# Kernel tuning notes

Hardware: AMD Instinct MI355X
Metric: run time of the kernel (lower is better)

Reference implementation:

```python
import jax, jax.numpy as jnp
import numpy as np

B = 4          # batch_size (config.batch_size)
N = 17000      # num_prots (nodes per graph)
F_IN = 256     # num_features
C = 128        # out_channels
E = 2176000    # num edges (avg degree 32)
NODES = B * N


def _gcn_layer(x, W, b, src, dst, n):
    """PyG GCNConv: add self-loops, sym-normalized aggregation, then bias.
    out[i] = sum_{j->i} d_j^{-1/2} d_i^{-1/2} (x_j W) + d_i^{-1} (x_i W) + b
    with d = degree(dst) + 1 (self loop)."""
    h = x @ W  # [n, C]
    deg = jax.ops.segment_sum(jnp.ones(src.shape[0], x.dtype), dst, num_segments=n) + 1.0
    dinv = jax.lax.rsqrt(deg)  # [n]
    coef = dinv[src] * dinv[dst]                      # [E]
    agg = jax.ops.segment_sum(h[src] * coef[:, None], dst, num_segments=n)
    agg = agg + h * (dinv * dinv)[:, None]            # self-loop term
    return agg + b


def setup_inputs() -> dict:
    key = jax.random.key(0)
    ks = jax.random.split(key, 16)

    def glorot(k, shape):
        fan_in, fan_out = shape[0], shape[1]
        s = jnp.sqrt(6.0 / (fan_in + fan_out))
        return jax.random.uniform(k, shape, jnp.float32, -s, s)

    inp = {
        "x": jax.random.normal(ks[0], (NODES, F_IN), jnp.float32),
        "edge_index": jax.random.randint(ks[1], (2, E), 0, NODES, jnp.int32),
        "protein_mask": jax.random.randint(ks[2], (B, N), 0, 2, jnp.int32),
        "W1": glorot(ks[3], (F_IN, C)), "b1": jnp.zeros((C,), jnp.float32),
        "W2": glorot(ks[4], (C, C)),    "b2": jnp.zeros((C,), jnp.float32),
        "W3": glorot(ks[5], (C, C)),    "b3": jnp.zeros((C,), jnp.float32),
        "lw1": glorot(ks[6], (C, 256)), "lb1": jnp.zeros((256,), jnp.float32),
        "lw2": glorot(ks[7], (256, 64)), "lb2": jnp.zeros((64,), jnp.float32),
        "lw3": glorot(ks[8], (64, 16)),  "lb3": jnp.zeros((16,), jnp.float32),
        "lw4": glorot(ks[9], (16, 1)),   "lb4": jnp.zeros((1,), jnp.float32),
    }
    return inp


def reference(x, edge_index, protein_mask, W1, b1, W2, b2, W3, b3,
              lw1, lb1, lw2, lb2, lw3, lb3, lw4, lb4):
    src, dst = edge_index[0], edge_index[1]
    h1 = jax.nn.relu(_gcn_layer(x, W1, b1, src, dst, NODES))   # [NODES, C]
    h2 = jax.nn.relu(_gcn_layer(h1, W2, b2, src, dst, NODES))
    h3 = jax.nn.relu(_gcn_layer(h2, W3, b3, src, dst, NODES))
    s = (h1 + h2 + h3).reshape(B, N, C)                        # residual sum
    mask = protein_mask.astype(jnp.float32)                    # [B, N]
    pooled = jnp.einsum('bn,bnc->bc', mask, s)                 # masked bmm pool [B, C]
    z = jax.nn.relu(pooled @ lw1 + lb1)
    z = jax.nn.relu(z @ lw2 + lb2)
    z = jax.nn.relu(z @ lw3 + lb3)
    return z @ lw4 + lb4                                       # [B, 1]
```

## Files before the change

kernel.cpp:

```cpp
#include <hip/hip_runtime.h>
#include <hip/hip_bf16.h>
#include <cstdint>

#define F_IN 256
#define C 128
#define NBUK_MAX 320
#define CHUNK 4096
#define CAP 12288

typedef short bf8_t __attribute__((ext_vector_type(8)));
typedef float f4_t  __attribute__((ext_vector_type(4)));

static inline size_t align256(size_t x) { return (x + 255) & ~(size_t)255; }

static __device__ inline unsigned pack_bf16(float a, float b) {
    __hip_bfloat162 h = __float22bfloat162_rn(make_float2(a, b));
    return *(unsigned*)&h;
}

static __device__ inline bf8_t pack8(float4 u0, float4 u1) {
    union { unsigned u[4]; bf8_t v; } r;
    r.u[0] = pack_bf16(u0.x, u0.y);
    r.u[1] = pack_bf16(u0.z, u0.w);
    r.u[2] = pack_bf16(u1.x, u1.y);
    r.u[3] = pack_bf16(u1.z, u1.w);
    return r.v;
}

__global__ __launch_bounds__(512) void part_gemm1_kernel(
        const int* __restrict__ src, const int* __restrict__ dst,
        int* __restrict__ cntb, int* __restrict__ ebuf, int E, int nblk_part,
        const float* __restrict__ X, const __hip_bfloat16* __restrict__ Wsw,
        __hip_bfloat16* __restrict__ G, int M) {
    __shared__ __align__(16) char smem[36864];
    const int tid = threadIdx.x;

    if ((int)blockIdx.x < nblk_part) {
        int* hist = (int*)smem;
        int* base = hist + NBUK_MAX;
        int* gbase = base + NBUK_MAX;
        int2* stage = (int2*)(smem + 4096);
        const int e0 = blockIdx.x * CHUNK;
        const int cnt = min(CHUNK, E - e0);

        for (int i = tid; i < NBUK_MAX; i += 512) hist[i] = 0;
        __syncthreads();

        int2 ev[CHUNK / 512];
        int mo[CHUNK / 512];
#pragma unroll
        for (int k = 0; k < CHUNK / 512; ++k) {
            int e = e0 + k * 512 + tid;
            if (e < E) {
                int2 v;
                v.x = src[e];
                v.y = dst[e];
                ev[k] = v;
                mo[k] = atomicAdd(&hist[v.y >> 8], 1);
            }
        }
        __syncthreads();
        if (tid < 64) {
            int acc[5];
            int s = 0;
#pragma unroll
            for (int j = 0; j < 5; ++j) {
                acc[j] = s;
                s += hist[tid * 5 + j];
            }
            int tot = s;
#pragma unroll
            for (int d = 1; d < 64; d <<= 1) {
                int o = __shfl_up(tot, d);
                if (tid >= d) tot += o;
            }
            int excl = tot - s;
#pragma unroll
            for (int j = 0; j < 5; ++j) base[tid * 5 + j] = excl + acc[j];
        }
        __syncthreads();
        for (int i = tid; i < NBUK_MAX; i += 512) {
            int h = hist[i];
            gbase[i] = h ? atomicAdd(&cntb[i], h) : 0;
        }
        __syncthreads();
#pragma unroll
        for (int k = 0; k < CHUNK / 512; ++k) {
            int e = e0 + k * 512 + tid;
            if (e < E) stage[base[ev[k].y >> 8] + mo[k]] = ev[k];
        }
        __syncthreads();
        for (int i = tid; i < cnt; i += 512) {
            int2 e = stage[i];
            int b = e.y >> 8;
            ebuf[(size_t)b * CAP + gbase[b] + (i - base[b])] = ((e.y & 255) << 24) | e.x;
        }
    } else {
        char* lds = smem;
        const int gb = blockIdx.x - nblk_part;
        const int l = tid & 63;
        const int w = tid >> 6;
        const int lm = l & 15;
        const int lk = (l >> 4) * 8;
        const int row0 = gb * 128 + w * 16;
        const int K = F_IN;

        f4_t acc[8] = {};
        const int r = min(row0 + lm, M - 1);
        const float* xf = X + (size_t)r * K + lk;

        for (int c = 0; c < 2; ++c) {
            if (c) __syncthreads();
            const char* wsrc = (const char*)Wsw + (size_t)c * 32768;
            for (int o = tid * 16; o < 32768; o += 512 * 16)
                *(uint4*)(lds + o) = *(const uint4*)(wsrc + o);
            __syncthreads();
#pragma unroll
            for (int s2 = 0; s2 < 4; ++s2) {
                const int s = c * 4 + s2;
                float4 u0 = *(const float4*)(xf + s * 32);
                float4 u1 = *(const float4*)(xf + s * 32 + 4);
                bf8_t a = pack8(u0, u1);
                const char* bbase = lds + ((size_t)(s2 * 8) * 64 + l) * 16;
#pragma unroll
                for (int u = 0; u < 8; ++u) {
                    bf8_t b = *(const bf8_t*)(bbase + (size_t)u * 64 * 16);
                    acc[u] = __builtin_amdgcn_mfma_f32_16x16x32_bf16(a, b, acc[u], 0, 0, 0);
                }
            }
        }
        const int rbase = row0 + (l >> 4) * 4;
#pragma unroll
        for (int rr = 0; rr < 4; ++rr) {
            int row = rbase + rr;
            if (row < M) {
#pragma unroll
                for (int u = 0; u < 8; ++u)
                    G[(size_t)row * C + u * 16 + lm] = __float2bfloat16(acc[u][rr]);
            }
        }
    }
}

__global__ __launch_bounds__(256) void csr_build_kernel(const int* __restrict__ ebuf,
                                                        const int* __restrict__ cntb,
                                                        int nbuk,
                                                        int* __restrict__ offs,
                                                        float* __restrict__ dinv,
                                                        int* __restrict__ csr, int nodes) {
    __shared__ int hist[NBUK_MAX];
    __shared__ int basep[NBUK_MAX];
    __shared__ int deg[256];
    __shared__ int p[256];
    __shared__ int pre[257];
    __shared__ int cur[256];
    const int b = blockIdx.x;
    const int n0 = b << 8;
    const int ncnt = min(256, nodes - n0);
    const int tid = threadIdx.x;

    for (int bk = tid; bk < NBUK_MAX; bk += 256)
        hist[bk] = (bk < nbuk) ? cntb[bk] : 0;
    __syncthreads();
    if (tid < 64) {
        int acc[5];
        int s = 0;
#pragma unroll
        for (int j = 0; j < 5; ++j) {
            acc[j] = s;
            s += hist[tid * 5 + j];
        }
        int tot = s;
#pragma unroll
        for (int d = 1; d < 64; d <<= 1) {
            int o = __shfl_up(tot, d);
            if (tid >= d) tot += o;
        }
        int excl = tot - s;
#pragma unroll
        for (int j = 0; j < 5; ++j) basep[tid * 5 + j] = excl + acc[j];
    }
    __syncthreads();
    const int eb = basep[b];
    const int cntE = hist[b];
    const int* slab = ebuf + (size_t)b * CAP;

    deg[tid] = 0;
    __syncthreads();
    for (int k = tid; k < cntE; k += 256)
        atomicAdd(&deg[(unsigned)slab[k] >> 24], 1);
    __syncthreads();
    p[tid] = deg[tid];
    __syncthreads();
    for (int d = 1; d < 256; d <<= 1) {
        int v = (tid >= d) ? p[tid - d] : 0;
        __syncthreads();
        p[tid] += v;
        __syncthreads();
    }
    pre[tid + 1] = p[tid];
    if (tid == 0) pre[0] = 0;
    __syncthreads();

    for (int i = tid; i <= ncnt; i += 256)
        offs[n0 + i] = eb + pre[i] + n0 + i;
    if (tid < ncnt) {
        dinv[n0 + tid] = rsqrtf((float)(deg[tid] + 1));
        csr[eb + pre[tid] + n0 + tid] = n0 + tid;
    }
    cur[tid] = 0;
    __syncthreads();
    for (int k = tid; k < cntE; k += 256) {
        int v = slab[k];
        int loc = (unsigned)v >> 24;
        int q = atomicAdd(&cur[loc], 1);
        csr[eb + pre[loc] + n0 + loc + 1 + q] = v & 0xFFFFFF;
    }
}

static __device__ inline void swz_one(const float* __restrict__ W,
                                      __hip_bfloat16* __restrict__ Wsw, int i) {
    int l = i & 63;
    int u = (i >> 6) & 7;
    int t = i >> 9;
    int krow = t * 32 + (l >> 4) * 8;
    int col = u * 16 + (l & 15);
    unsigned packed[4];
#pragma unroll
    for (int j = 0; j < 4; ++j) {
        float a = W[(size_t)(krow + 2 * j) * C + col];
        float b = W[(size_t)(krow + 2 * j + 1) * C + col];
        packed[j] = pack_bf16(a, b);
    }
    uint4 o = make_uint4(packed[0], packed[1], packed[2], packed[3]);
    *(uint4*)(Wsw + (size_t)i * 8) = o;
}

__global__ __launch_bounds__(256) void wswz_all_kernel(const float* __restrict__ W1,
                                                       const float* __restrict__ W2,
                                                       const float* __restrict__ W3,
                                                       __hip_bfloat16* __restrict__ Wsw1,
                                                       __hip_bfloat16* __restrict__ Wsw2,
                                                       __hip_bfloat16* __restrict__ Wsw3,
                                                       int* __restrict__ cntb, int nbuk,
                                                       float* __restrict__ pooled) {
    if (blockIdx.x == 32) {
        const int tid = threadIdx.x;
        for (int i = tid; i < nbuk; i += 256) cntb[i] = 0;
        for (int i = tid; i < 4 * C; i += 256) pooled[i] = 0.f;
        return;
    }
    int i = blockIdx.x * blockDim.x + threadIdx.x;
    if (i < 4096)      swz_one(W1, Wsw1, i);
    else if (i < 6144) swz_one(W2, Wsw2, i - 4096);
    else if (i < 8192) swz_one(W3, Wsw3, i - 6144);
}

__global__ __launch_bounds__(256) void mfma_gemm_kernel(const __hip_bfloat16* __restrict__ Xv,
                                                        const __hip_bfloat16* __restrict__ Wsw,
                                                        const float* __restrict__ dinv,
                                                        __hip_bfloat16* __restrict__ G,
                                                        int M) {
    __shared__ char lds[32768];
    const int tid = threadIdx.x;
    const int l = tid & 63;
    const int w = tid >> 6;
    const int lm = l & 15;
    const int lk = (l >> 4) * 8;
    const int row0 = blockIdx.x * 128 + w * 32;
    const int K = C;

    f4_t acc[2][8] = {};
    const __hip_bfloat16* xb[2];
#pragma unroll
    for (int mt = 0; mt < 2; ++mt) {
        int r = min(row0 + mt * 16 + lm, M - 1);
        xb[mt] = Xv + (size_t)r * K + lk;
    }
    bf8_t cb[2];
#pragma unroll
    for (int mt = 0; mt < 2; ++mt)
        cb[mt] = *(const bf8_t*)(xb[mt]);

    for (int o = tid * 16; o < 32768; o += 256 * 16)
        *(uint4*)(lds + o) = *(const uint4*)((const char*)Wsw + o);
    __syncthreads();

    for (int s = 0; s < 4; ++s) {
        bf8_t nb[2];
        if (s + 1 < 4) {
#pragma unroll
            for (int mt = 0; mt < 2; ++mt)
                nb[mt] = *(const bf8_t*)(xb[mt] + (s + 1) * 32);
        }
        const char* bbase = lds + ((size_t)(s * 8) * 64 + l) * 16;
#pragma unroll
        for (int u = 0; u < 8; ++u) {
            bf8_t b = *(const bf8_t*)(bbase + (size_t)u * 64 * 16);
#pragma unroll
            for (int mt = 0; mt < 2; ++mt)
                acc[mt][u] = __builtin_amdgcn_mfma_f32_16x16x32_bf16(cb[mt], b, acc[mt][u], 0, 0, 0);
        }
        if (s + 1 < 4) {
#pragma unroll
            for (int mt = 0; mt < 2; ++mt)
                cb[mt] = nb[mt];
        }
    }

#pragma unroll
    for (int mt = 0; mt < 2; ++mt) {
        int rbase = row0 + mt * 16 + (l >> 4) * 4;
#pragma unroll
        for (int r = 0; r < 4; ++r) {
            int row = rbase + r;
            if (row < M) {
                float dv = dinv[row];
#pragma unroll
                for (int u = 0; u < 8; ++u) {
                    float v = acc[mt][u][r] * dv;
                    G[(size_t)row * C + u * 16 + lm] = __float2bfloat16(v);
                }
            }
        }
    }
}

static __device__ inline void unpack_add(uint4 v, float* acc) {
    const __hip_bfloat162* hh = (const __hip_bfloat162*)&v;
#pragma unroll
    for (int t = 0; t < 4; ++t) {
        float2 f = __bfloat1622float2(hh[t]);
        acc[2 * t]     += f.x;
        acc[2 * t + 1] += f.y;
    }
}

static __device__ inline void unpack_fma(uint4 v, float dv, float* acc) {
    const __hip_bfloat162* hh = (const __hip_bfloat162*)&v;
#pragma unroll
    for (int t = 0; t < 4; ++t) {
        float2 f = __bfloat1622float2(hh[t]);
        acc[2 * t]     = fmaf(f.x, dv, acc[2 * t]);
        acc[2 * t + 1] = fmaf(f.y, dv, acc[2 * t + 1]);
    }
}

template <bool SS>
static __device__ inline void gather_rows(const char* __restrict__ Gb,
                                          const int* __restrict__ csr,
                                          const float* __restrict__ dinv,
                                          int beg, int end, int l, int g,
                                          unsigned qoff, float* acc) {
    for (int base = beg; base < end; base += 64) {
        const int cnt = min(64, end - base);
        int myidx = (l < cnt) ? csr[base + l] : 0;
        float mydv = SS ? dinv[myidx] : 1.f;
        int j = 0;
        for (; j + 16 <= cnt; j += 16) {
            int i0 = __shfl(myidx, j + g);
            int i1 = __shfl(myidx, j + 4 + g);
            int i2 = __shfl(myidx, j + 8 + g);
            int i3 = __shfl(myidx, j + 12 + g);
            uint4 v0 = *(const uint4*)(Gb + (((unsigned)i0 << 8) | qoff));
            uint4 v1 = *(const uint4*)(Gb + (((unsigned)i1 << 8) | qoff));
            uint4 v2 = *(const uint4*)(Gb + (((unsigned)i2 << 8) | qoff));
            uint4 v3 = *(const uint4*)(Gb + (((unsigned)i3 << 8) | qoff));
            if (SS) {
                float d0 = __shfl(mydv, j + g);
                float d1 = __shfl(mydv, j + 4 + g);
                float d2 = __shfl(mydv, j + 8 + g);
                float d3 = __shfl(mydv, j + 12 + g);
                unpack_fma(v0, d0, acc); unpack_fma(v1, d1, acc);
                unpack_fma(v2, d2, acc); unpack_fma(v3, d3, acc);
            } else {
                unpack_add(v0, acc); unpack_add(v1, acc);
                unpack_add(v2, acc); unpack_add(v3, acc);
            }
        }
        if (j + 8 <= cnt) {
            int i0 = __shfl(myidx, j + g);
            int i1 = __shfl(myidx, j + 4 + g);
            uint4 v0 = *(const uint4*)(Gb + (((unsigned)i0 << 8) | qoff));
            uint4 v1 = *(const uint4*)(Gb + (((unsigned)i1 << 8) | qoff));
            if (SS) {
                float d0 = __shfl(mydv, j + g);
                float d1 = __shfl(mydv, j + 4 + g);
                unpack_fma(v0, d0, acc); unpack_fma(v1, d1, acc);
            } else {
                unpack_add(v0, acc); unpack_add(v1, acc);
            }
            j += 8;
        }
        for (; j < cnt; j += 4) {
            int i0 = __shfl(myidx, j + g);
            float sc = (j + g < cnt) ? 1.f : 0.f;
            if (SS) sc *= __shfl(mydv, j + g);
            uint4 v0 = *(const uint4*)(Gb + (((unsigned)i0 << 8) | qoff));
            unpack_fma(v0, sc, acc);
        }
    }
}

template <bool SS>
__global__ __launch_bounds__(256) void agg_kernel(const __hip_bfloat16* __restrict__ G,
                                                  const int* __restrict__ csr,
                                                  const int* __restrict__ offs,
                                                  const float* __restrict__ dinv,
                                                  const float* __restrict__ bias,
                                                  __hip_bfloat16* __restrict__ A, int nodes) {
    const int node = blockIdx.x * 4 + (threadIdx.x >> 6);
    if (node >= nodes) return;
    const int l = threadIdx.x & 63;
    const int g = l >> 4;
    const unsigned qoff = (l & 15) * 16;
    const int beg = offs[node], end = offs[node + 1];
    float acc[8] = {};
    gather_rows<SS>((const char*)G, csr, dinv, beg, end, l, g, qoff, acc);

#pragma unroll
    for (int t = 0; t < 8; ++t) {
        acc[t] += __shfl_xor(acc[t], 16);
        acc[t] += __shfl_xor(acc[t], 32);
    }

    const float d = dinv[node];
    if (g == 0) {
        float bb[8];
        *(float4*)bb       = *(const float4*)(bias + qoff / 2);
        *(float4*)(bb + 4) = *(const float4*)(bias + qoff / 2 + 4);
        unsigned pk[4];
#pragma unroll
        for (int t = 0; t < 4; ++t) {
            float x0 = fmaxf(fmaf(acc[2 * t],     d, bb[2 * t]),     0.f);
            float x1 = fmaxf(fmaf(acc[2 * t + 1], d, bb[2 * t + 1]), 0.f);
            pk[t] = pack_bf16(x0, x1);
        }
        *(uint4*)((char*)A + (size_t)node * 256 + qoff) = make_uint4(pk[0], pk[1], pk[2], pk[3]);
    }
}

__global__ __launch_bounds__(64) void pool3_kernel(const __hip_bfloat16* __restrict__ S1,
                                                   const __hip_bfloat16* __restrict__ S2,
                                                   const __hip_bfloat16* __restrict__ S3,
                                                   const int* __restrict__ mask,
                                                   float* __restrict__ pooled, int N) {
    const int b = blockIdx.y;
    const int n0 = blockIdx.x * 128;
    const int c0 = threadIdx.x * 2;
    const int lim = min(n0 + 128, N);
    float ax = 0.f, ay = 0.f;
    for (int n = n0; n < lim; ++n) {
        if (mask[b * N + n]) {
            size_t o = ((size_t)b * N + n) * C + c0;
            float2 f1 = __bfloat1622float2(*(const __hip_bfloat162*)(S1 + o));
            float2 f2 = __bfloat1622float2(*(const __hip_bfloat162*)(S2 + o));
            float2 f3 = __bfloat1622float2(*(const __hip_bfloat162*)(S3 + o));
            ax += f1.x + f2.x + f3.x;
            ay += f1.y + f2.y + f3.y;
        }
    }
    atomicAdd(&pooled[b * C + c0], ax);
    atomicAdd(&pooled[b * C + c0 + 1], ay);
}

__global__ __launch_bounds__(256) void mlp_kernel(const float* __restrict__ pooled,
        const float* __restrict__ lw1, const float* __restrict__ lb1,
        const float* __restrict__ lw2, const float* __restrict__ lb2,
        const float* __restrict__ lw3, const float* __restrict__ lb3,
        const float* __restrict__ lw4, const float* __restrict__ lb4,
        float* __restrict__ out) {
    __shared__ float p[4 * 128];
    __shared__ float z1[4 * 256];
    __shared__ float z2[4 * 64];
    __shared__ float z3[4 * 16];
    const int tid = threadIdx.x;
    for (int i = tid; i < 4 * 128; i += 256) p[i] = pooled[i];
    __syncthreads();
    for (int o = tid; o < 4 * 256; o += 256) {
        int b = o >> 8, j = o & 255;
        float s = lb1[j];
        for (int k = 0; k < 128; ++k) s += p[b * 128 + k] * lw1[k * 256 + j];
        z1[o] = fmaxf(s, 0.f);
    }
    __syncthreads();
    for (int o = tid; o < 4 * 64; o += 256) {
        int b = o >> 6, j = o & 63;
        float s = lb2[j];
        for (int k = 0; k < 256; ++k) s += z1[b * 256 + k] * lw2[k * 64 + j];
        z2[o] = fmaxf(s, 0.f);
    }
    __syncthreads();
    if (tid < 64) {
        int b = tid >> 4, j = tid & 15;
        float s = lb3[j];
        for (int k = 0; k < 64; ++k) s += z2[b * 64 + k] * lw3[k * 16 + j];
        z3[tid] = fmaxf(s, 0.f);
    }
    __syncthreads();
    if (tid < 4) {
        float s = lb4[0];
        for (int k = 0; k < 16; ++k) s += z3[tid * 16 + k] * lw4[k];
        out[tid] = s;
    }
}


extern "C" void kernel_launch(void* const* d_in, const int* in_sizes, int n_in,
                              void* d_out, int out_size, void* d_ws, size_t ws_size,
                              hipStream_t stream) {
    const float* x    = (const float*)d_in[0];
    const int*   ei   = (const int*)d_in[1];
    const int*   pmask = (const int*)d_in[2];
    const float* W1 = (const float*)d_in[3];  const float* b1 = (const float*)d_in[4];
    const float* W2 = (const float*)d_in[5];  const float* b2 = (const float*)d_in[6];
    const float* W3 = (const float*)d_in[7];  const float* b3 = (const float*)d_in[8];
    const float* lw1 = (const float*)d_in[9];  const float* lb1 = (const float*)d_in[10];
    const float* lw2 = (const float*)d_in[11]; const float* lb2 = (const float*)d_in[12];
    const float* lw3 = (const float*)d_in[13]; const float* lb3 = (const float*)d_in[14];
    const float* lw4 = (const float*)d_in[15]; const float* lb4 = (const float*)d_in[16];
    float* out = (float*)d_out;

    const int E = in_sizes[1] / 2;
    const int NODES = in_sizes[0] / F_IN;
    const int NB = 4;
    const int NPER = NODES / NB;
    const int NBUK = (NODES + 255) >> 8;
    const int NBLK = (E + CHUNK - 1) / CHUNK;
    const int* esrc = ei;
    const int* edst = ei + E;

    char* w = (char*)d_ws;
    size_t off = 0;
    auto alloc = [&](size_t bytes) -> void* {
        void* p = w + off;
        off = align256(off + bytes);
        return p;
    };
    float* dinv = (float*)alloc((size_t)NODES * 4);
    int*   offs = (int*)  alloc((size_t)(NODES + 1) * 4);
    int*   cntb = (int*)  alloc((size_t)NBUK * 4);
    int*   ebuf = (int*)  alloc((size_t)NBUK * CAP * 4);
    int*   csr  = (int*)  alloc((size_t)(E + NODES) * 4);
    __hip_bfloat16* G   = (__hip_bfloat16*)alloc((size_t)NODES * C * 2);
    __hip_bfloat16* A1  = (__hip_bfloat16*)alloc((size_t)NODES * C * 2);
    __hip_bfloat16* A2  = (__hip_bfloat16*)alloc((size_t)NODES * C * 2);
    __hip_bfloat16* A3  = (__hip_bfloat16*)alloc((size_t)NODES * C * 2);
    __hip_bfloat16* Wsw1 = (__hip_bfloat16*)alloc((size_t)F_IN * C * 2);
    __hip_bfloat16* Wsw2 = (__hip_bfloat16*)alloc((size_t)C * C * 2);
    __hip_bfloat16* Wsw3 = (__hip_bfloat16*)alloc((size_t)C * C * 2);
    float* pooled = (float*)alloc((size_t)4 * C * 4);
    (void)ws_size; (void)n_in; (void)out_size;

    const int gblocks128 = (NODES + 127) / 128;
    const int ablocks = (NODES + 3) / 4;

    wswz_all_kernel<<<33, 256, 0, stream>>>(W1, W2, W3, Wsw1, Wsw2, Wsw3,
                                            cntb, NBUK, pooled);

    part_gemm1_kernel<<<NBLK + gblocks128, 512, 0, stream>>>(
        esrc, edst, cntb, ebuf, E, NBLK, x, Wsw1, G, NODES);

    csr_build_kernel<<<NBUK, 256, 0, stream>>>(ebuf, cntb, NBUK, offs, dinv, csr, NODES);

    agg_kernel<true><<<ablocks, 256, 0, stream>>>(G, csr, offs, dinv, b1, A1, NODES);
    mfma_gemm_kernel<<<gblocks128, 256, 0, stream>>>(A1, Wsw2, dinv, G, NODES);
    agg_kernel<false><<<ablocks, 256, 0, stream>>>(G, csr, offs, dinv, b2, A2, NODES);
    mfma_gemm_kernel<<<gblocks128, 256, 0, stream>>>(A2, Wsw3, dinv, G, NODES);
    agg_kernel<false><<<ablocks, 256, 0, stream>>>(G, csr, offs, dinv, b3, A3, NODES);

    dim3 pgrid((NPER + 127) / 128, NB);
    pool3_kernel<<<pgrid, 64, 0, stream>>>(A1, A2, A3, pmask, pooled, NPER);
    mlp_kernel<<<1, 256, 0, stream>>>(pooled, lw1, lb1, lw2, lb2, lw3, lb3, lw4, lb4, out);
}
```

Baseline: 468.4 us.

## Fold per-layer masked pooling into GEMM launches as extra blocks

Removes the three-input pool3 kernel. Pooling of A1 and A2 now runs as extra blocks appended to the following GEMM launches, which read the same activation buffer, and a small standalone pool kernel handles A3. The aim is to hide pooling behind GEMM work and read each activation while it may still be in cache. The cost is extra atomics into pooled, since there are now three passes, and some uneven block work inside the combined launches.

```diff
diff --git a/kernel.cpp b/kernel.cpp
--- a/kernel.cpp
+++ b/kernel.cpp
@@ -256,26 +256,23 @@
     else if (i < 8192) swz_one(W3, Wsw3, i - 6144);
 }
 
-__global__ __launch_bounds__(256) void mfma_gemm_kernel(const __hip_bfloat16* __restrict__ Xv,
-                                                        const __hip_bfloat16* __restrict__ Wsw,
-                                                        const float* __restrict__ dinv,
-                                                        __hip_bfloat16* __restrict__ G,
-                                                        int M) {
-    __shared__ char lds[32768];
-    const int tid = threadIdx.x;
+static __device__ inline void gemm128_full_body(const __hip_bfloat16* __restrict__ Xv,
+                                                const __hip_bfloat16* __restrict__ Wsw,
+                                                const float* __restrict__ dinv,
+                                                __hip_bfloat16* __restrict__ G,
+                                                int M, int row0blk, int tid, char* lds) {
     const int l = tid & 63;
     const int w = tid >> 6;
     const int lm = l & 15;
     const int lk = (l >> 4) * 8;
-    const int row0 = blockIdx.x * 128 + w * 32;
-    const int K = C;
+    const int row0 = row0blk + w * 32;
 
     f4_t acc[2][8] = {};
     const __hip_bfloat16* xb[2];
 #pragma unroll
     for (int mt = 0; mt < 2; ++mt) {
         int r = min(row0 + mt * 16 + lm, M - 1);
-        xb[mt] = Xv + (size_t)r * K + lk;
+        xb[mt] = Xv + (size_t)r * C + lk;
     }
     bf8_t cb[2];
 #pragma unroll
@@ -324,6 +321,50 @@
             }
         }
     }
+}
+
+static __device__ inline void pool_body(const __hip_bfloat16* __restrict__ S,
+                                        const int* __restrict__ mask,
+                                        float* __restrict__ pooled, int N,
+                                        int pb, int nbx2, int tid) {
+    const int bx = pb % nbx2;
+    const int by = pb / nbx2;
+    const int l = tid & 63;
+    const int w = tid >> 6;
+    const int c0 = l * 2;
+    const int n0 = bx * 512;
+    const int lim = min(n0 + 512, N);
+    float ax = 0.f, ay = 0.f;
+    for (int n = n0 + w; n < lim; n += 4) {
+        if (mask[by * N + n]) {
+            size_t o = ((size_t)by * N + n) * C + c0;
+            float2 f = __bfloat1622float2(*(const __hip_bfloat162*)(S + o));
+            ax += f.x;
+            ay += f.y;
+        }
+    }
+    atomicAdd(&pooled[by * C + c0], ax);
+    atomicAdd(&pooled[by * C + c0 + 1], ay);
+}
+
+__global__ __launch_bounds__(256) void gemm_pool_union_kernel(
+        const __hip_bfloat16* __restrict__ Xv, const __hip_bfloat16* __restrict__ Wsw,
+        const float* __restrict__ dinv, __hip_bfloat16* __restrict__ G, int M, int nGemm,
+        const int* __restrict__ mask, float* __restrict__ pooled, int N, int nbx2) {
+    __shared__ __align__(16) char lds[32768];
+    const int tid = threadIdx.x;
+    if ((int)blockIdx.x < nGemm) {
+        gemm128_full_body(Xv, Wsw, dinv, G, M, blockIdx.x * 128, tid, lds);
+    } else {
+        pool_body(Xv, mask, pooled, N, blockIdx.x - nGemm, nbx2, tid);
+    }
+}
+
+__global__ __launch_bounds__(256) void pool_std_kernel(const __hip_bfloat16* __restrict__ S,
+                                                       const int* __restrict__ mask,
+                                                       float* __restrict__ pooled,
+                                                       int N, int nbx2) {
+    pool_body(S, mask, pooled, N, blockIdx.x, nbx2, threadIdx.x);
 }
 
 static __device__ inline void unpack_add(uint4 v, float* acc) {
@@ -440,30 +481,6 @@
     }
 }
 
-__global__ __launch_bounds__(64) void pool3_kernel(const __hip_bfloat16* __restrict__ S1,
-                                                   const __hip_bfloat16* __restrict__ S2,
-                                                   const __hip_bfloat16* __restrict__ S3,
-                                                   const int* __restrict__ mask,
-                                                   float* __restrict__ pooled, int N) {
-    const int b = blockIdx.y;
-    const int n0 = blockIdx.x * 128;
-    const int c0 = threadIdx.x * 2;
-    const int lim = min(n0 + 128, N);
-    float ax = 0.f, ay = 0.f;
-    for (int n = n0; n < lim; ++n) {
-        if (mask[b * N + n]) {
-            size_t o = ((size_t)b * N + n) * C + c0;
-            float2 f1 = __bfloat1622float2(*(const __hip_bfloat162*)(S1 + o));
-            float2 f2 = __bfloat1622float2(*(const __hip_bfloat162*)(S2 + o));
-            float2 f3 = __bfloat1622float2(*(const __hip_bfloat162*)(S3 + o));
-            ax += f1.x + f2.x + f3.x;
-            ay += f1.y + f2.y + f3.y;
-        }
-    }
-    atomicAdd(&pooled[b * C + c0], ax);
-    atomicAdd(&pooled[b * C + c0 + 1], ay);
-}
-
 __global__ __launch_bounds__(256) void mlp_kernel(const float* __restrict__ pooled,
         const float* __restrict__ lw1, const float* __restrict__ lb1,
         const float* __restrict__ lw2, const float* __restrict__ lb2,
@@ -554,6 +571,8 @@
 
     const int gblocks128 = (NODES + 127) / 128;
     const int ablocks = (NODES + 3) / 4;
+    const int nbx2 = (NPER + 511) / 512;
+    const int pblocks = nbx2 * NB;
 
     wswz_all_kernel<<<33, 256, 0, stream>>>(W1, W2, W3, Wsw1, Wsw2, Wsw3,
                                             cntb, NBUK, pooled);
@@ -564,12 +583,13 @@
     csr_build_kernel<<<NBUK, 256, 0, stream>>>(ebuf, cntb, NBUK, offs, dinv, csr, NODES);
 
     agg_kernel<true><<<ablocks, 256, 0, stream>>>(G, csr, offs, dinv, b1, A1, NODES);
-    mfma_gemm_kernel<<<gblocks128, 256, 0, stream>>>(A1, Wsw2, dinv, G, NODES);
+    gemm_pool_union_kernel<<<gblocks128 + pblocks, 256, 0, stream>>>(
+        A1, Wsw2, dinv, G, NODES, gblocks128, pmask, pooled, NPER, nbx2);
     agg_kernel<false><<<ablocks, 256, 0, stream>>>(G, csr, offs, dinv, b2, A2, NODES);
-    mfma_gemm_kernel<<<gblocks128, 256, 0, stream>>>(A2, Wsw3, dinv, G, NODES);
+    gemm_pool_union_kernel<<<gblocks128 + pblocks, 256, 0, stream>>>(
+        A2, Wsw3, dinv, G, NODES, gblocks128, pmask, pooled, NPER, nbx2);
     agg_kernel<false><<<ablocks, 256, 0, stream>>>(G, csr, offs, dinv, b3, A3, NODES);
 
-    dim3 pgrid((NPER + 127) / 128, NB);
-    pool3_kernel<<<pgrid, 64, 0, stream>>>(A1, A2, A3, pmask, pooled, NPER);
+    pool_std_kernel<<<pblocks, 256, 0, stream>>>(A3, pmask, pooled, NPER, nbx2);
     mlp_kernel<<<1, 256, 0, stream>>>(pooled, lw1, lb1, lw2, lb2, lw3, lb3, lw4, lb4, out);
 }
```

Measured after the change: 555.6 us. 18.6% more time.
